# Kernel optimization log

Hardware: AMD Instinct MI355X
Metric: run time of the kernel (lower is better)

## Reference

```python
import jax, jax.numpy as jnp
import numpy as np

N_NODES = 4096
DEG_HALF = 16
MAX_E = 64
D = 128
H = 4
L = 2
N_SPECIES = 4
R_CUT = 5.0
R_TRANS = 3.0


def _layer_norm(x, w, b, eps=1e-5):
    m = jnp.mean(x, axis=-1, keepdims=True)
    v = jnp.mean((x - m) ** 2, axis=-1, keepdims=True)
    return (x - m) * jax.lax.rsqrt(v + eps) * w + b


def _transformer(x, radial_mask, p):
    # x: (N, MAX_E, D); radial_mask: (N, MAX_E). Pre-LN transformer whose
    # attention weights are reweighted by the radial cutoff mask over keys.
    ln1_w, ln1_b, qkv_w, qkv_b, out_w, out_b, ln2_w, ln2_b, m1_w, m1_b, m2_w, m2_b = p
    n, s, d = x.shape
    dh = d // H
    scale = np.float32(1.0 / np.sqrt(dh))
    for l in range(L):
        h = _layer_norm(x, ln1_w[l], ln1_b[l])
        qkv = h @ qkv_w[l] + qkv_b[l]  # (n, s, 3d)
        q, k, v = jnp.split(qkv, 3, axis=-1)
        q = q.reshape(n, s, H, dh).transpose(0, 2, 1, 3)
        k = k.reshape(n, s, H, dh).transpose(0, 2, 1, 3)
        v = v.reshape(n, s, H, dh).transpose(0, 2, 1, 3)
        a = jax.nn.softmax(jnp.einsum("nhqc,nhkc->nhqk", q, k) * scale, axis=-1)
        a = a * radial_mask[:, None, None, :]
        a = a / (jnp.sum(a, axis=-1, keepdims=True) + 1e-9)
        o = jnp.einsum("nhqk,nhkc->nhqc", a, v).transpose(0, 2, 1, 3).reshape(n, s, d)
        x = x + o @ out_w[l] + out_b[l]
        h = _layer_norm(x, ln2_w[l], ln2_b[l])
        x = x + jax.nn.gelu(h @ m1_w[l] + m1_b[l]) @ m2_w[l] + m2_b[l]
    return x


def _forward(edge_vectors, enc_cart_w, enc_center_emb, enc_neighbor_emb, enc_comp_w,
             t0, t1, gnn_w, last_w, comp_w,
             species_index, centers, neighbors, nef_indices, nef_mask,
             nef_to_edges_neighbor, corresponding_edges):
    r = jnp.sqrt(jnp.sum(edge_vectors ** 2, axis=-1))
    radial = jnp.where(r < R_TRANS, 1.0,
                       0.5 * (jnp.cos(jnp.pi * (r - R_TRANS) / (R_CUT - R_TRANS)) + 1.0))
    radial = jnp.where(r < R_CUT, radial, 0.0)
    eic = species_index[centers]
    ein = species_index[neighbors]
    # edge_array_to_nef gathers
    ev_nef = edge_vectors[nef_indices]                  # (N, MAX_E, 3)
    rm = jnp.where(nef_mask, radial[nef_indices], 0.0)  # (N, MAX_E)
    enc = jnp.concatenate([ev_nef @ enc_cart_w,
                           enc_center_emb[eic[nef_indices]],
                           enc_neighbor_emb[ein[nef_indices]]], axis=-1)
    feat = enc @ enc_comp_w                             # (N, MAX_E, D)
    feat = _transformer(feat, rm, t0)
    # one message-passing round (num_gnn_layers=2 -> 1 MP layer)
    edge_feat = feat[centers, nef_to_edges_neighbor]    # NEF -> edge list, (E, D)
    new = jnp.concatenate([edge_feat, edge_feat[corresponding_edges]], axis=-1) @ gnn_w
    new = _transformer(new[nef_indices], rm, t1)        # edge list -> NEF
    feat = feat + new
    node_features = jnp.sum(feat * rm[..., None], axis=1)  # masked scatter-sum
    return node_features @ last_w + comp_w[species_index][:, None]  # (N, 1)


def setup_inputs() -> dict:
    rng = np.random.default_rng(0)
    src = np.repeat(np.arange(N_NODES), DEG_HALF)
    dst = (src + rng.integers(1, N_NODES, size=src.shape[0])) % N_NODES
    centers = np.concatenate([src, dst]).astype(np.int64)
    neighbors = np.concatenate([dst, src]).astype(np.int64)
    E = centers.shape[0]
    corresponding_edges = np.concatenate([np.arange(E // 2, E), np.arange(E // 2)]).astype(np.int64)
    order = np.argsort(centers, kind="stable")
    sc = centers[order]
    starts = np.searchsorted(sc, np.arange(N_NODES))
    ranks = np.arange(E) - starts[sc]
    assert ranks.max() < MAX_E
    nef_indices = np.zeros((N_NODES, MAX_E), np.int64)
    nef_mask = np.zeros((N_NODES, MAX_E), bool)
    nef_indices[sc, ranks] = order
    nef_mask[sc, ranks] = True
    nef_to_edges_neighbor = np.zeros(E, np.int64)
    nef_to_edges_neighbor[order] = ranks
    half = rng.standard_normal((E // 2, 3)) * 1.6
    edge_vectors = np.concatenate([half, -half]).astype(np.float32)
    species_index = rng.integers(0, N_SPECIES, N_NODES).astype(np.int64)

    keys = iter(jax.random.split(jax.random.key(0), 80))

    def lin(shape, fan_in):
        return jax.random.normal(next(keys), shape, jnp.float32) / np.float32(np.sqrt(fan_in))

    inp = {
        "edge_vectors": jnp.asarray(edge_vectors),
        "enc_cart_w": lin((3, D), 3),
        "enc_center_emb": lin((N_SPECIES, D), 1),
        "enc_neighbor_emb": lin((N_SPECIES, D), 1),
        "enc_comp_w": lin((3 * D, D), 3 * D),
        "gnn_w": lin((2 * D, D), 2 * D),
        "last_w": lin((D, 1), D),
        "comp_w": lin((N_SPECIES,), 1),
        "species_index": jnp.asarray(species_index),
        "centers": jnp.asarray(centers),
        "neighbors": jnp.asarray(neighbors),
        "nef_indices": jnp.asarray(nef_indices),
        "nef_mask": jnp.asarray(nef_mask),
        "nef_to_edges_neighbor": jnp.asarray(nef_to_edges_neighbor),
        "corresponding_edges": jnp.asarray(corresponding_edges),
    }
    for t in ("t0", "t1"):
        inp[t + "_ln1_w"] = jnp.ones((L, D), jnp.float32)
        inp[t + "_ln1_b"] = jnp.zeros((L, D), jnp.float32)
        inp[t + "_qkv_w"] = lin((L, D, 3 * D), D)
        inp[t + "_qkv_b"] = jnp.zeros((L, 3 * D), jnp.float32)
        inp[t + "_out_w"] = lin((L, D, D), D)
        inp[t + "_out_b"] = jnp.zeros((L, D), jnp.float32)
        inp[t + "_ln2_w"] = jnp.ones((L, D), jnp.float32)
        inp[t + "_ln2_b"] = jnp.zeros((L, D), jnp.float32)
        inp[t + "_mlp1_w"] = lin((L, D, 4 * D), D)
        inp[t + "_mlp1_b"] = jnp.zeros((L, 4 * D), jnp.float32)
        inp[t + "_mlp2_w"] = lin((L, 4 * D, D), 4 * D)
        inp[t + "_mlp2_b"] = jnp.zeros((L, D), jnp.float32)
    return inp


def reference(edge_vectors, enc_cart_w, enc_center_emb, enc_neighbor_emb, enc_comp_w,
              t0_ln1_w, t0_ln1_b, t0_qkv_w, t0_qkv_b, t0_out_w, t0_out_b,
              t0_ln2_w, t0_ln2_b, t0_mlp1_w, t0_mlp1_b, t0_mlp2_w, t0_mlp2_b,
              t1_ln1_w, t1_ln1_b, t1_qkv_w, t1_qkv_b, t1_out_w, t1_out_b,
              t1_ln2_w, t1_ln2_b, t1_mlp1_w, t1_mlp1_b, t1_mlp2_w, t1_mlp2_b,
              gnn_w, last_w, comp_w,
              species_index, centers, neighbors, nef_indices, nef_mask,
              nef_to_edges_neighbor, corresponding_edges):
    t0 = (t0_ln1_w, t0_ln1_b, t0_qkv_w, t0_qkv_b, t0_out_w, t0_out_b,
          t0_ln2_w, t0_ln2_b, t0_mlp1_w, t0_mlp1_b, t0_mlp2_w, t0_mlp2_b)
    t1 = (t1_ln1_w, t1_ln1_b, t1_qkv_w, t1_qkv_b, t1_out_w, t1_out_b,
          t1_ln2_w, t1_ln2_b, t1_mlp1_w, t1_mlp1_b, t1_mlp2_w, t1_mlp2_b)
    return _forward(edge_vectors, enc_cart_w, enc_center_emb, enc_neighbor_emb, enc_comp_w,
                    t0, t1, gnn_w, last_w, comp_w,
                    species_index, centers, neighbors, nef_indices, nef_mask,
                    nef_to_edges_neighbor, corresponding_edges)
```

## Files before the change

### kernel.cpp

```cpp
#include <hip/hip_runtime.h>

typedef short s8v __attribute__((ext_vector_type(8)));
typedef float f4v __attribute__((ext_vector_type(4)));

#define MFMA16(a,b,c) __builtin_amdgcn_mfma_f32_16x16x32_bf16((a),(b),(c),0,0,0)

#define N_NODES 4096
#define N_EDGE  131072
#define ATT_SCALE 0.17677669529663687f
#define GELU_C   0.7978845608028654f

__device__ __forceinline__ unsigned short f2bf(float f) {
  union { float f; unsigned u; } v; v.f = f;
  unsigned r = v.u + 0x7fffu + ((v.u >> 16) & 1u);
  return (unsigned short)(r >> 16);
}
__device__ __forceinline__ float bf2f(short s) {
  union { unsigned u; float f; } v;
  v.u = ((unsigned)(unsigned short)s) << 16;
  return v.f;
}
__device__ __forceinline__ int iclamp(int v, int lo, int hi) {
  return v < lo ? lo : (v > hi ? hi : v);
}


__global__ void k_tr(const float* __restrict__ src, short* __restrict__ dst,
                     int L, int K, int N) {
  int idx = blockIdx.x * 256 + threadIdx.x;
  int tot = L * K * N;
  if (idx >= tot) return;
  int l = idx / (K * N);
  int r = idx - l * (K * N);
  int k = r / N;
  int n = r - k * N;
  dst[l * K * N + n * K + k] = (short)f2bf(src[idx]);
}

__global__ void k_tabs(const float* __restrict__ cart, const float* __restrict__ cemb,
                       const float* __restrict__ nemb, const float* __restrict__ comp,
                       float* __restrict__ tabs) {
  int idx = blockIdx.x * 256 + threadIdx.x;
  if (idx >= 1408) return;
  float s = 0.f;
  if (idx < 384) {
    int i = idx >> 7, d = idx & 127;
    for (int j = 0; j < 128; ++j) s += cart[i * 128 + j] * comp[j * 128 + d];
  } else if (idx < 896) {
    int i2 = idx - 384; int sp = i2 >> 7, d = i2 & 127;
    for (int j = 0; j < 128; ++j) s += cemb[sp * 128 + j] * comp[(128 + j) * 128 + d];
  } else {
    int i2 = idx - 896; int sp = i2 >> 7, d = i2 & 127;
    for (int j = 0; j < 128; ++j) s += nemb[sp * 128 + j] * comp[(256 + j) * 128 + d];
  }
  tabs[idx] = s;
}

__global__ void k_rm(const float* __restrict__ ev, const int* __restrict__ centers,
                     const int* __restrict__ nef2, float* __restrict__ rm) {
  int e = blockIdx.x * 256 + threadIdx.x;
  if (e >= N_EDGE) return;
  float x = ev[e*3], y = ev[e*3+1], z = ev[e*3+2];
  float r = sqrtf(x*x + y*y + z*z);
  float rad;
  if (r < 3.0f)      rad = 1.0f;
  else if (r < 5.0f) rad = 0.5f * (cosf(3.14159265358979f * (r - 3.0f) * 0.5f) + 1.0f);
  else               rad = 0.0f;
  int c  = iclamp(centers[e], 0, N_NODES - 1);
  int rk = iclamp(nef2[e], 0, 63);
  rm[c * 64 + rk] = rad;
}

__global__ __launch_bounds__(256) void k_enc(
    const float* __restrict__ ev, const int* __restrict__ nef,
    const int* __restrict__ centers, const int* __restrict__ neighbors,
    const int* __restrict__ species, const float* __restrict__ tabs,
    short* __restrict__ feat) {
  int n = blockIdx.x, t = threadIdx.x, j = t >> 2, qq = t & 3;
  int e = iclamp(nef[n * 64 + j], 0, N_EDGE - 1);
  float e0 = ev[e*3], e1 = ev[e*3+1], e2 = ev[e*3+2];
  int nc = iclamp(centers[e],   0, N_NODES - 1);
  int nn = iclamp(neighbors[e], 0, N_NODES - 1);
  int sc = iclamp(species[nc], 0, 3), sn = iclamp(species[nn], 0, 3);
  const float* m0 = tabs + qq*32;
  const float* m1 = tabs + 128 + qq*32;
  const float* m2 = tabs + 256 + qq*32;
  const float* tc = tabs + 384 + sc*128 + qq*32;
  const float* tn = tabs + 896 + sn*128 + qq*32;
  short* o = feat + ((size_t)(n*64 + j))*128 + qq*32;
  #pragma unroll
  for (int i = 0; i < 32; i += 2) {
    float a = e0*m0[i]   + e1*m1[i]   + e2*m2[i]   + tc[i]   + tn[i];
    float b = e0*m0[i+1] + e1*m1[i+1] + e2*m2[i+1] + tc[i+1] + tn[i+1];
    *(unsigned*)(o + i) = (unsigned)f2bf(a) | ((unsigned)f2bf(b) << 16);
  }
}


__device__ __forceinline__ void ln_sub(float (&xr)[4][2][4],
                                       const float* __restrict__ gw, const float* __restrict__ gb,
                                       float* red, short* hb, int wid, int quad, int l4) {
  #pragma unroll
  for (int mt = 0; mt < 4; ++mt)
    #pragma unroll
    for (int reg = 0; reg < 4; ++reg) {
      float a = xr[mt][0][reg] + xr[mt][1][reg];
      float s = xr[mt][0][reg]*xr[mt][0][reg] + xr[mt][1][reg]*xr[mt][1][reg];
      #pragma unroll
      for (int m = 1; m < 16; m <<= 1) { a += __shfl_xor(a, m); s += __shfl_xor(s, m); }
      if (l4 == 0) {
        int r = mt*16 + quad*4 + reg;
        red[(wid*64 + r)*2]     = a;
        red[(wid*64 + r)*2 + 1] = s;
      }
    }
  __syncthreads();
  int tid = threadIdx.x;
  if (tid < 64) {
    float a = 0.f, s = 0.f;
    #pragma unroll
    for (int w = 0; w < 4; ++w) { a += red[(w*64 + tid)*2]; s += red[(w*64 + tid)*2 + 1]; }
    float mean = a * (1.f/128.f);
    float var  = s * (1.f/128.f) - mean*mean;
    red[tid*2]     = mean;
    red[tid*2 + 1] = rsqrtf(var + 1e-5f);
  }
  __syncthreads();
  float gv[2], bv[2];
  #pragma unroll
  for (int nt = 0; nt < 2; ++nt) { int c = wid*32 + nt*16 + l4; gv[nt] = gw[c]; bv[nt] = gb[c]; }
  #pragma unroll
  for (int mt = 0; mt < 4; ++mt)
    #pragma unroll
    for (int reg = 0; reg < 4; ++reg) {
      int r = mt*16 + quad*4 + reg;
      float mean = red[r*2], inv = red[r*2 + 1];
      #pragma unroll
      for (int nt = 0; nt < 2; ++nt) {
        float h = (xr[mt][nt][reg] - mean) * inv * gv[nt] + bv[nt];
        hb[r*136 + wid*32 + nt*16 + l4] = (short)f2bf(h);
      }
    }
  __syncthreads();
}

__global__ __launch_bounds__(256, 2) void k_tf(
    short* __restrict__ x, const float* __restrict__ rm,
    const float* __restrict__ lnw1, const float* __restrict__ lnb1,
    const short* __restrict__ qkvT, const float* __restrict__ qkvb,
    const short* __restrict__ outT, const float* __restrict__ outb,
    const float* __restrict__ lnw2, const float* __restrict__ lnb2,
    const short* __restrict__ m1T, const float* __restrict__ m1b,
    const short* __restrict__ m2T, const float* __restrict__ m2b) {
  __shared__ __align__(16) char smem[55552];
  short* hb  = (short*)smem;
  short* kb  = (short*)(smem + 17408);
  short* vtb = (short*)(smem + 34816);
  float* red = (float*)(smem + 53248);
  float* rmb = (float*)(smem + 55296);

  const int tid = threadIdx.x;
  const int wid = tid >> 6;
  const int lane = tid & 63;
  const int l4 = lane & 15;
  const int quad = lane >> 4;
  const int n = blockIdx.x;

  if (tid < 64) rmb[tid] = rm[n*64 + tid];

  short* xg = x + (size_t)n * 64 * 128;
  float xr[4][2][4];
  #pragma unroll
  for (int mt = 0; mt < 4; ++mt)
    #pragma unroll
    for (int nt = 0; nt < 2; ++nt)
      #pragma unroll
      for (int reg = 0; reg < 4; ++reg)
        xr[mt][nt][reg] = bf2f(xg[(mt*16 + quad*4 + reg)*128 + wid*32 + nt*16 + l4]);

  for (int l = 0; l < 2; ++l) {
    const float* g1    = lnw1 + l*128;   const float* bb1   = lnb1 + l*128;
    const short* qkvTl = qkvT + l*49152; const float* qkvbl = qkvb + l*384;
    const short* outTl = outT + l*16384; const float* outbl = outb + l*128;
    const float* g2    = lnw2 + l*128;   const float* bb2   = lnb2 + l*128;
    const short* m1Tl  = m1T + l*65536;  const float* m1bl  = m1b + l*512;
    const short* m2Tl  = m2T + l*65536;  const float* m2bl  = m2b + l*128;

    ln_sub(xr, g1, bb1, red, hb, wid, quad, l4);

    {
      s8v af[4][4];
      #pragma unroll
      for (int mt = 0; mt < 4; ++mt)
        #pragma unroll
        for (int k0 = 0; k0 < 4; ++k0)
          af[mt][k0] = *(const s8v*)(hb + (mt*16 + l4)*136 + k0*32 + quad*8);
      __syncthreads();

      for (int j = 0; j < 6; ++j) {
        int col = wid*96 + j*16 + l4;
        s8v bf[4];
        #pragma unroll
        for (int k0 = 0; k0 < 4; ++k0)
          bf[k0] = *(const s8v*)(qkvTl + col*128 + k0*32 + quad*8);
        float bias = qkvbl[col];
        f4v acc[4];
        #pragma unroll
        for (int mt = 0; mt < 4; ++mt) { f4v zz = {0.f,0.f,0.f,0.f}; acc[mt] = zz; }
        #pragma unroll
        for (int k0 = 0; k0 < 4; ++k0)
          #pragma unroll
          for (int mt = 0; mt < 4; ++mt)
            acc[mt] = MFMA16(af[mt][k0], bf[k0], acc[mt]);
        if (col < 128) {
          #pragma unroll
          for (int mt = 0; mt < 4; ++mt)
            #pragma unroll
            for (int reg = 0; reg < 4; ++reg)
              hb[(mt*16 + quad*4 + reg)*136 + col] = (short)f2bf((acc[mt][reg] + bias) * ATT_SCALE);
        } else if (col < 256) {
          int c = col - 128;
          #pragma unroll
          for (int mt = 0; mt < 4; ++mt)
            #pragma unroll
            for (int reg = 0; reg < 4; ++reg)
              kb[(mt*16 + quad*4 + reg)*136 + c] = (short)f2bf(acc[mt][reg] + bias);
        } else {
          int c = col - 256;
          #pragma unroll
          for (int mt = 0; mt < 4; ++mt)
            #pragma unroll
            for (int reg = 0; reg < 4; ++reg)
              vtb[c*72 + (mt*16 + quad*4 + reg)] = (short)f2bf(acc[mt][reg] + bias);
        }
      }
    }
    __syncthreads();

    {
      const int h = wid;
      s8v aq[4], bk[4];
      #pragma unroll
      for (int mt = 0; mt < 4; ++mt)
        aq[mt] = *(const s8v*)(hb + (mt*16 + l4)*136 + h*32 + quad*8);
      #pragma unroll
      for (int n2 = 0; n2 < 4; ++n2)
        bk[n2] = *(const s8v*)(kb + (n2*16 + l4)*136 + h*32 + quad*8);
      f4v S[4][4];
      #pragma unroll
      for (int mt = 0; mt < 4; ++mt)
        #pragma unroll
        for (int n2 = 0; n2 < 4; ++n2) {
          f4v zz = {0.f,0.f,0.f,0.f};
          S[mt][n2] = MFMA16(aq[mt], bk[n2], zz);
        }
      __syncthreads();

      float rv[4];
      #pragma unroll
      for (int n2 = 0; n2 < 4; ++n2) rv[n2] = rmb[n2*16 + l4];
      #pragma unroll
      for (int mt = 0; mt < 4; ++mt)
        #pragma unroll
        for (int reg = 0; reg < 4; ++reg) {
          float mx = fmaxf(fmaxf(S[mt][0][reg], S[mt][1][reg]),
                           fmaxf(S[mt][2][reg], S[mt][3][reg]));
          mx = fmaxf(mx, __shfl_xor(mx, 1));
          mx = fmaxf(mx, __shfl_xor(mx, 2));
          mx = fmaxf(mx, __shfl_xor(mx, 4));
          mx = fmaxf(mx, __shfl_xor(mx, 8));
          float E = 0.f, W = 0.f;
          #pragma unroll
          for (int n2 = 0; n2 < 4; ++n2) {
            float e = __expf(S[mt][n2][reg] - mx);
            E += e; W += e * rv[n2];
            S[mt][n2][reg] = e * rv[n2];
          }
          E += __shfl_xor(E, 1); E += __shfl_xor(E, 2);
          E += __shfl_xor(E, 4); E += __shfl_xor(E, 8);
          W += __shfl_xor(W, 1); W += __shfl_xor(W, 2);
          W += __shfl_xor(W, 4); W += __shfl_xor(W, 8);
          float inv = 1.f / (W + 1e-9f * E);
          #pragma unroll
          for (int n2 = 0; n2 < 4; ++n2) S[mt][n2][reg] *= inv;
        }

      short* pt = kb + wid * 2048;
      f4v o[4][2];
      #pragma unroll
      for (int mt = 0; mt < 4; ++mt)
        #pragma unroll
        for (int nt = 0; nt < 2; ++nt) { f4v zz = {0.f,0.f,0.f,0.f}; o[mt][nt] = zz; }
      for (int c = 0; c < 2; ++c) {
        #pragma unroll
        for (int mt = 0; mt < 4; ++mt)
          #pragma unroll
          for (int n2 = 0; n2 < 2; ++n2)
            #pragma unroll
            for (int reg = 0; reg < 4; ++reg)
              pt[(mt*16 + quad*4 + reg)*32 + n2*16 + l4] = (short)f2bf(S[mt][2*c + n2][reg]);
        s8v ap[4];
        #pragma unroll
        for (int mt = 0; mt < 4; ++mt)
          ap[mt] = *(const s8v*)(pt + (mt*16 + l4)*32 + quad*8);
        #pragma unroll
        for (int nt = 0; nt < 2; ++nt) {
          s8v bv = *(const s8v*)(vtb + (h*32 + nt*16 + l4)*72 + c*32 + quad*8);
          #pragma unroll
          for (int mt = 0; mt < 4; ++mt)
            o[mt][nt] = MFMA16(ap[mt], bv, o[mt][nt]);
        }
      }
      #pragma unroll
      for (int mt = 0; mt < 4; ++mt)
        #pragma unroll
        for (int nt = 0; nt < 2; ++nt)
          #pragma unroll
          for (int reg = 0; reg < 4; ++reg)
            hb[(mt*16 + quad*4 + reg)*136 + h*32 + nt*16 + l4] = (short)f2bf(o[mt][nt][reg]);
    }
    __syncthreads();

    {
      s8v ao[4][4];
      #pragma unroll
      for (int mt = 0; mt < 4; ++mt)
        #pragma unroll
        for (int k0 = 0; k0 < 4; ++k0)
          ao[mt][k0] = *(const s8v*)(hb + (mt*16 + l4)*136 + k0*32 + quad*8);
      #pragma unroll
      for (int nt = 0; nt < 2; ++nt) {
        int c = wid*32 + nt*16 + l4;
        s8v bo[4];
        #pragma unroll
        for (int k0 = 0; k0 < 4; ++k0)
          bo[k0] = *(const s8v*)(outTl + c*128 + k0*32 + quad*8);
        float bias = outbl[c];
        #pragma unroll
        for (int mt = 0; mt < 4; ++mt) {
          f4v a2 = {xr[mt][nt][0], xr[mt][nt][1], xr[mt][nt][2], xr[mt][nt][3]};
          #pragma unroll
          for (int k0 = 0; k0 < 4; ++k0)
            a2 = MFMA16(ao[mt][k0], bo[k0], a2);
          #pragma unroll
          for (int reg = 0; reg < 4; ++reg)
            xr[mt][nt][reg] = a2[reg] + bias;
        }
      }
    }

    ln_sub(xr, g2, bb2, red, hb, wid, quad, l4);

    {
      s8v afm[4][4];
      #pragma unroll
      for (int mt = 0; mt < 4; ++mt)
        #pragma unroll
        for (int k0 = 0; k0 < 4; ++k0)
          afm[mt][k0] = *(const s8v*)(hb + (mt*16 + l4)*136 + k0*32 + quad*8);
      __syncthreads();

      for (int cc = 0; cc < 4; ++cc) {
        #pragma unroll
        for (int nt = 0; nt < 2; ++nt) {
          int jc = cc*128 + wid*32 + nt*16 + l4;
          s8v bm[4];
          #pragma unroll
          for (int k0 = 0; k0 < 4; ++k0)
            bm[k0] = *(const s8v*)(m1Tl + jc*128 + k0*32 + quad*8);
          float bias = m1bl[jc];
          #pragma unroll
          for (int mt = 0; mt < 4; ++mt) {
            f4v a2 = {0.f,0.f,0.f,0.f};
            #pragma unroll
            for (int k0 = 0; k0 < 4; ++k0)
              a2 = MFMA16(afm[mt][k0], bm[k0], a2);
            #pragma unroll
            for (int reg = 0; reg < 4; ++reg) {
              float v = a2[reg] + bias;
              float zz2 = GELU_C * (v + 0.044715f * v * v * v);
              float ee = __expf(2.f * zz2);
              float th = 1.f - 2.f / (ee + 1.f);
              float gl = 0.5f * v * (1.f + th);
              hb[(mt*16 + quad*4 + reg)*136 + wid*32 + nt*16 + l4] = (short)f2bf(gl);
            }
          }
        }
        __syncthreads();
        s8v at4[4][4];
        #pragma unroll
        for (int mt = 0; mt < 4; ++mt)
          #pragma unroll
          for (int k0 = 0; k0 < 4; ++k0)
            at4[mt][k0] = *(const s8v*)(hb + (mt*16 + l4)*136 + k0*32 + quad*8);
        #pragma unroll
        for (int nt = 0; nt < 2; ++nt) {
          int c = wid*32 + nt*16 + l4;
          s8v b2f[4];
          #pragma unroll
          for (int k0 = 0; k0 < 4; ++k0)
            b2f[k0] = *(const s8v*)(m2Tl + c*512 + cc*128 + k0*32 + quad*8);
          #pragma unroll
          for (int mt = 0; mt < 4; ++mt) {
            f4v a2 = {xr[mt][nt][0], xr[mt][nt][1], xr[mt][nt][2], xr[mt][nt][3]};
            #pragma unroll
            for (int k0 = 0; k0 < 4; ++k0)
              a2 = MFMA16(at4[mt][k0], b2f[k0], a2);
            #pragma unroll
            for (int reg = 0; reg < 4; ++reg)
              xr[mt][nt][reg] = a2[reg];
          }
        }
        __syncthreads();
      }
      #pragma unroll
      for (int nt = 0; nt < 2; ++nt) {
        float b = m2bl[wid*32 + nt*16 + l4];
        #pragma unroll
        for (int mt = 0; mt < 4; ++mt)
          #pragma unroll
          for (int reg = 0; reg < 4; ++reg)
            xr[mt][nt][reg] += b;
      }
    }
  }

  #pragma unroll
  for (int mt = 0; mt < 4; ++mt)
    #pragma unroll
    for (int nt = 0; nt < 2; ++nt)
      #pragma unroll
      for (int reg = 0; reg < 4; ++reg)
        xg[(mt*16 + quad*4 + reg)*128 + wid*32 + nt*16 + l4] = (short)f2bf(xr[mt][nt][reg]);
}

__global__ __launch_bounds__(256) void k_gnn(
    const short* __restrict__ feat, const int* __restrict__ nef,
    const int* __restrict__ corr, const int* __restrict__ centers,
    const int* __restrict__ nef2, const short* __restrict__ gnnT,
    short* __restrict__ out) {
  __shared__ __align__(16) short Ab[64 * 264];
  int n = blockIdx.x, t = threadIdx.x;
  int wid = t >> 6, lane = t & 63, l4 = lane & 15, quad = lane >> 4;
  int j = t >> 2, qq = t & 3;
  int e  = iclamp(nef[n*64 + j], 0, N_EDGE - 1);
  int ce = iclamp(corr[e], 0, N_EDGE - 1);
  size_t r1 = ((size_t)iclamp(centers[e],  0, N_NODES-1) * 64 + iclamp(nef2[e],  0, 63)) * 128;
  size_t r2 = ((size_t)iclamp(centers[ce], 0, N_NODES-1) * 64 + iclamp(nef2[ce], 0, 63)) * 128;
  {
    const s8v* p1 = (const s8v*)(feat + r1 + qq*32);
    const s8v* p2 = (const s8v*)(feat + r2 + qq*32);
    #pragma unroll
    for (int ii = 0; ii < 4; ++ii) {
      *(s8v*)(Ab + j*264 + qq*32 + ii*8)       = p1[ii];
      *(s8v*)(Ab + j*264 + 128 + qq*32 + ii*8) = p2[ii];
    }
  }
  __syncthreads();
  f4v acc[4][2];
  #pragma unroll
  for (int mt = 0; mt < 4; ++mt)
    #pragma unroll
    for (int nt = 0; nt < 2; ++nt) { f4v zz = {0.f,0.f,0.f,0.f}; acc[mt][nt] = zz; }
  #pragma unroll
  for (int k0 = 0; k0 < 8; ++k0) {
    s8v a[4];
    #pragma unroll
    for (int mt = 0; mt < 4; ++mt)
      a[mt] = *(const s8v*)(Ab + (mt*16 + l4)*264 + k0*32 + quad*8);
    #pragma unroll
    for (int nt = 0; nt < 2; ++nt) {
      s8v b = *(const s8v*)(gnnT + (wid*32 + nt*16 + l4)*256 + k0*32 + quad*8);
      #pragma unroll
      for (int mt = 0; mt < 4; ++mt)
        acc[mt][nt] = MFMA16(a[mt], b, acc[mt][nt]);
    }
  }
  #pragma unroll
  for (int mt = 0; mt < 4; ++mt)
    #pragma unroll
    for (int nt = 0; nt < 2; ++nt)
      #pragma unroll
      for (int reg = 0; reg < 4; ++reg)
        out[((size_t)n*64 + mt*16 + quad*4 + reg)*128 + wid*32 + nt*16 + l4] =
            (short)f2bf(acc[mt][nt][reg]);
}

__global__ __launch_bounds__(256) void k_final(
    const short* __restrict__ feat, const short* __restrict__ buf2,
    const float* __restrict__ rm, const float* __restrict__ lastw,
    const float* __restrict__ compw, const int* __restrict__ species,
    float* __restrict__ out) {
  __shared__ float part[4];
  int n = blockIdx.x, t = threadIdx.x;
  int wid = t >> 6, lane = t & 63;
  int j = t >> 2, qq = t & 3;
  size_t base = ((size_t)n*64 + j)*128 + qq*32;
  float s = 0.f;
  #pragma unroll
  for (int i = 0; i < 32; ++i)
    s += (bf2f(feat[base + i]) + bf2f(buf2[base + i])) * lastw[qq*32 + i];
  s += __shfl_xor(s, 1);
  s += __shfl_xor(s, 2);
  float v = (qq == 0) ? s * rm[n*64 + j] : 0.f;
  v += __shfl_xor(v, 4);  v += __shfl_xor(v, 8);
  v += __shfl_xor(v, 16); v += __shfl_xor(v, 32);
  if (lane == 0) part[wid] = v;
  __syncthreads();
  if (t == 0) out[n] = part[0] + part[1] + part[2] + part[3]
                       + compw[iclamp(species[n], 0, 3)];
}


extern "C" void kernel_launch(void* const* d_in, const int* in_sizes, int n_in,
                              void* d_out, int out_size, void* d_ws, size_t ws_size,
                              hipStream_t stream) {
  const float* ev      = (const float*)d_in[0];
  const float* cart    = (const float*)d_in[1];
  const float* cemb    = (const float*)d_in[2];
  const float* nemb    = (const float*)d_in[3];
  const float* comp    = (const float*)d_in[4];
  const float* gnnw    = (const float*)d_in[5];
  const float* lastw   = (const float*)d_in[6];
  const float* compw   = (const float*)d_in[7];
  const int*   species = (const int*)d_in[8];
  const int*   centers = (const int*)d_in[9];
  const int*   neighbors = (const int*)d_in[10];
  const int*   nef     = (const int*)d_in[11];
  const int*   nef2    = (const int*)d_in[13];
  const int*   corr    = (const int*)d_in[14];

  const size_t OFF_RM   = 0;
  const size_t OFF_FEAT = 1048576;
  const size_t OFF_BUF2 = 68157440;
  const size_t OFF_TABS = 135266304;
  const size_t OFF_WBF  = 135271936;
  const size_t NEED     = 136910336;
  if (ws_size < NEED) return;

  char* ws = (char*)d_ws;
  float* rm   = (float*)(ws + OFF_RM);
  short* feat = (short*)(ws + OFF_FEAT);
  short* buf2 = (short*)(ws + OFF_BUF2);
  float* tabs = (float*)(ws + OFF_TABS);
  short* wbf  = (short*)(ws + OFF_WBF);

  short* t0q  = wbf + 0;
  short* t0o  = wbf + 98304;
  short* t0m1 = wbf + 131072;
  short* t0m2 = wbf + 262144;
  short* t1q  = wbf + 393216;
  short* t1o  = wbf + 491520;
  short* t1m1 = wbf + 524288;
  short* t1m2 = wbf + 655360;
  short* gnnT = wbf + 786432;

  hipMemsetAsync(rm, 0, 4096*64*sizeof(float), stream);

  k_tr<<<384, 256, 0, stream>>>((const float*)d_in[17], t0q,  2, 128, 384);
  k_tr<<<128, 256, 0, stream>>>((const float*)d_in[19], t0o,  2, 128, 128);
  k_tr<<<512, 256, 0, stream>>>((const float*)d_in[23], t0m1, 2, 128, 512);
  k_tr<<<512, 256, 0, stream>>>((const float*)d_in[25], t0m2, 2, 512, 128);
  k_tr<<<384, 256, 0, stream>>>((const float*)d_in[29], t1q,  2, 128, 384);
  k_tr<<<128, 256, 0, stream>>>((const float*)d_in[31], t1o,  2, 128, 128);
  k_tr<<<512, 256, 0, stream>>>((const float*)d_in[35], t1m1, 2, 128, 512);
  k_tr<<<512, 256, 0, stream>>>((const float*)d_in[37], t1m2, 2, 512, 128);
  k_tr<<<128, 256, 0, stream>>>(gnnw, gnnT, 1, 256, 128);
  k_tabs<<<6, 256, 0, stream>>>(cart, cemb, nemb, comp, tabs);
  k_rm<<<512, 256, 0, stream>>>(ev, centers, nef2, rm);
  k_enc<<<4096, 256, 0, stream>>>(ev, nef, centers, neighbors, species, tabs, feat);

  k_tf<<<4096, 256, 0, stream>>>(feat, rm,
      (const float*)d_in[15], (const float*)d_in[16], t0q, (const float*)d_in[18],
      t0o, (const float*)d_in[20], (const float*)d_in[21], (const float*)d_in[22],
      t0m1, (const float*)d_in[24], t0m2, (const float*)d_in[26]);

  k_gnn<<<4096, 256, 0, stream>>>(feat, nef, corr, centers, nef2, gnnT, buf2);

  k_tf<<<4096, 256, 0, stream>>>(buf2, rm,
      (const float*)d_in[27], (const float*)d_in[28], t1q, (const float*)d_in[30],
      t1o, (const float*)d_in[32], (const float*)d_in[33], (const float*)d_in[34],
      t1m1, (const float*)d_in[36], t1m2, (const float*)d_in[38]);

  k_final<<<4096, 256, 0, stream>>>(feat, buf2, rm, lastw, compw, species, (float*)d_out);
}
```

Baseline: 1.789 ms.

## Shrink transformer LDS footprint, double-buffer MLP tiles, and raise occupancy target

Cuts the fused transformer kernel's shared memory by keeping the radial mask in registers and reusing the V region for the reduction buffer. Launch bounds move from 2 to 3 blocks per CU. The MLP hidden tile now alternates between the K and V buffers so one barrier per chunk can go, and the m2 weight loads are issued before the barrier. It also switches the hot-path bf16 conversion to cheaper round-half-up, keeping round-to-nearest-even for weights and features, and partially unrolls the QKV loop. The higher occupancy target may force register spills, and the rounding change slightly alters numerics.

Result: slower. 1.832 ms (+2.4%).

```diff
diff --git a/kernel.cpp b/kernel.cpp
--- a/kernel.cpp
+++ b/kernel.cpp
@@ -11,6 +11,10 @@
 #define GELU_C   0.7978845608028654f
 
 __device__ __forceinline__ unsigned short f2bf(float f) {
+  union { float f; unsigned u; } v; v.f = f;
+  return (unsigned short)((v.u + 0x8000u) >> 16);
+}
+__device__ __forceinline__ unsigned short f2bf_rne(float f) {
   union { float f; unsigned u; } v; v.f = f;
   unsigned r = v.u + 0x7fffu + ((v.u >> 16) & 1u);
   return (unsigned short)(r >> 16);
@@ -34,7 +38,7 @@
   int r = idx - l * (K * N);
   int k = r / N;
   int n = r - k * N;
-  dst[l * K * N + n * K + k] = (short)f2bf(src[idx]);
+  dst[l * K * N + n * K + k] = (short)f2bf_rne(src[idx]);
 }
 
 __global__ void k_tabs(const float* __restrict__ cart, const float* __restrict__ cemb,
@@ -92,7 +96,7 @@
   for (int i = 0; i < 32; i += 2) {
     float a = e0*m0[i]   + e1*m1[i]   + e2*m2[i]   + tc[i]   + tn[i];
     float b = e0*m0[i+1] + e1*m1[i+1] + e2*m2[i+1] + tc[i+1] + tn[i+1];
-    *(unsigned*)(o + i) = (unsigned)f2bf(a) | ((unsigned)f2bf(b) << 16);
+    *(unsigned*)(o + i) = (unsigned)f2bf_rne(a) | ((unsigned)f2bf_rne(b) << 16);
   }
 }
 
@@ -144,7 +148,7 @@
   __syncthreads();
 }
 
-__global__ __launch_bounds__(256, 2) void k_tf(
+__global__ __launch_bounds__(256, 3) void k_tf(
     short* __restrict__ x, const float* __restrict__ rm,
     const float* __restrict__ lnw1, const float* __restrict__ lnb1,
     const short* __restrict__ qkvT, const float* __restrict__ qkvb,
@@ -152,12 +156,11 @@
     const float* __restrict__ lnw2, const float* __restrict__ lnb2,
     const short* __restrict__ m1T, const float* __restrict__ m1b,
     const short* __restrict__ m2T, const float* __restrict__ m2b) {
-  __shared__ __align__(16) char smem[55552];
+  __shared__ __align__(16) char smem[53248];
   short* hb  = (short*)smem;
   short* kb  = (short*)(smem + 17408);
   short* vtb = (short*)(smem + 34816);
-  float* red = (float*)(smem + 53248);
-  float* rmb = (float*)(smem + 55296);
+  float* red = (float*)(smem + 34816);
 
   const int tid = threadIdx.x;
   const int wid = tid >> 6;
@@ -166,7 +169,9 @@
   const int quad = lane >> 4;
   const int n = blockIdx.x;
 
-  if (tid < 64) rmb[tid] = rm[n*64 + tid];
+  float rv[4];
+  #pragma unroll
+  for (int n2 = 0; n2 < 4; ++n2) rv[n2] = rm[n*64 + n2*16 + l4];
 
   short* xg = x + (size_t)n * 64 * 128;
   float xr[4][2][4];
@@ -186,6 +191,8 @@
     const short* m1Tl  = m1T + l*65536;  const float* m1bl  = m1b + l*512;
     const short* m2Tl  = m2T + l*65536;  const float* m2bl  = m2b + l*128;
 
+    __syncthreads();
+
     ln_sub(xr, g1, bb1, red, hb, wid, quad, l4);
 
     {
@@ -197,6 +204,7 @@
           af[mt][k0] = *(const s8v*)(hb + (mt*16 + l4)*136 + k0*32 + quad*8);
       __syncthreads();
 
+      #pragma unroll 2
       for (int j = 0; j < 6; ++j) {
         int col = wid*96 + j*16 + l4;
         s8v bf[4];
@@ -254,11 +262,7 @@
           f4v zz = {0.f,0.f,0.f,0.f};
           S[mt][n2] = MFMA16(aq[mt], bk[n2], zz);
         }
-      __syncthreads();
-
-      float rv[4];
-      #pragma unroll
-      for (int n2 = 0; n2 < 4; ++n2) rv[n2] = rmb[n2*16 + l4];
+
       #pragma unroll
       for (int mt = 0; mt < 4; ++mt)
         #pragma unroll
@@ -285,7 +289,6 @@
           for (int n2 = 0; n2 < 4; ++n2) S[mt][n2][reg] *= inv;
         }
 
-      short* pt = kb + wid * 2048;
       f4v o[4][2];
       #pragma unroll
       for (int mt = 0; mt < 4; ++mt)
@@ -298,11 +301,12 @@
           for (int n2 = 0; n2 < 2; ++n2)
             #pragma unroll
             for (int reg = 0; reg < 4; ++reg)
-              pt[(mt*16 + quad*4 + reg)*32 + n2*16 + l4] = (short)f2bf(S[mt][2*c + n2][reg]);
+              kb[(mt*16 + quad*4 + reg)*136 + h*32 + n2*16 + l4] =
+                  (short)f2bf(S[mt][2*c + n2][reg]);
         s8v ap[4];
         #pragma unroll
         for (int mt = 0; mt < 4; ++mt)
-          ap[mt] = *(const s8v*)(pt + (mt*16 + l4)*32 + quad*8);
+          ap[mt] = *(const s8v*)(kb + (mt*16 + l4)*136 + h*32 + quad*8);
         #pragma unroll
         for (int nt = 0; nt < 2; ++nt) {
           s8v bv = *(const s8v*)(vtb + (h*32 + nt*16 + l4)*72 + c*32 + quad*8);
@@ -358,9 +362,9 @@
         #pragma unroll
         for (int k0 = 0; k0 < 4; ++k0)
           afm[mt][k0] = *(const s8v*)(hb + (mt*16 + l4)*136 + k0*32 + quad*8);
-      __syncthreads();
 
       for (int cc = 0; cc < 4; ++cc) {
+        short* G = (cc & 1) ? vtb : kb;
         #pragma unroll
         for (int nt = 0; nt < 2; ++nt) {
           int jc = cc*128 + wid*32 + nt*16 + l4;
@@ -382,36 +386,38 @@
               float ee = __expf(2.f * zz2);
               float th = 1.f - 2.f / (ee + 1.f);
               float gl = 0.5f * v * (1.f + th);
-              hb[(mt*16 + quad*4 + reg)*136 + wid*32 + nt*16 + l4] = (short)f2bf(gl);
+              G[(mt*16 + quad*4 + reg)*136 + wid*32 + nt*16 + l4] = (short)f2bf(gl);
             }
           }
         }
+        s8v b2f[2][4];
+        #pragma unroll
+        for (int nt = 0; nt < 2; ++nt) {
+          int c = wid*32 + nt*16 + l4;
+          #pragma unroll
+          for (int k0 = 0; k0 < 4; ++k0)
+            b2f[nt][k0] = *(const s8v*)(m2Tl + c*512 + cc*128 + k0*32 + quad*8);
+        }
         __syncthreads();
         s8v at4[4][4];
         #pragma unroll
         for (int mt = 0; mt < 4; ++mt)
           #pragma unroll
           for (int k0 = 0; k0 < 4; ++k0)
-            at4[mt][k0] = *(const s8v*)(hb + (mt*16 + l4)*136 + k0*32 + quad*8);
+            at4[mt][k0] = *(const s8v*)(G + (mt*16 + l4)*136 + k0*32 + quad*8);
         #pragma unroll
         for (int nt = 0; nt < 2; ++nt) {
-          int c = wid*32 + nt*16 + l4;
-          s8v b2f[4];
-          #pragma unroll
-          for (int k0 = 0; k0 < 4; ++k0)
-            b2f[k0] = *(const s8v*)(m2Tl + c*512 + cc*128 + k0*32 + quad*8);
           #pragma unroll
           for (int mt = 0; mt < 4; ++mt) {
             f4v a2 = {xr[mt][nt][0], xr[mt][nt][1], xr[mt][nt][2], xr[mt][nt][3]};
             #pragma unroll
             for (int k0 = 0; k0 < 4; ++k0)
-              a2 = MFMA16(at4[mt][k0], b2f[k0], a2);
+              a2 = MFMA16(at4[mt][k0], b2f[nt][k0], a2);
             #pragma unroll
             for (int reg = 0; reg < 4; ++reg)
               xr[mt][nt][reg] = a2[reg];
           }
         }
-        __syncthreads();
       }
       #pragma unroll
       for (int nt = 0; nt < 2; ++nt) {
```
